# Kernel tuning notes

Hardware: AMD Instinct MI355X
Metric: run time of the kernel (lower is better)

## Reference

```python
import jax, jax.numpy as jnp
import numpy as np

BN_EPS = 1e-5


def setup_inputs() -> dict:
    key = jax.random.key(0)
    ks = jax.random.split(key, 10)
    N, E, D = 100000, 1600000, 64
    node_feats = jax.random.normal(ks[0], (N, D), dtype=jnp.float32)
    edge_feats = jax.random.randint(ks[1], (E, 3), 0, 2, dtype=jnp.int64)
    edge_index = jax.random.randint(ks[2], (2, E), 0, N, dtype=jnp.int64)
    return {
        "node_feats": node_feats,
        "edge_feats": edge_feats,
        "edge_index": edge_index,
        "num_nodes": N,
        "num_edges": E,
        "eps": jnp.zeros((1,), jnp.float32),
        "bond_emb0": jax.random.normal(ks[3], (5, D), dtype=jnp.float32) * 0.05,
        "bond_emb1": jax.random.normal(ks[4], (6, D), dtype=jnp.float32) * 0.05,
        "bond_emb2": jax.random.normal(ks[5], (2, D), dtype=jnp.float32) * 0.05,
        "W1": jax.random.normal(ks[6], (2 * D, D), dtype=jnp.float32) * (1.0 / np.sqrt(D)),
        "b1": jnp.zeros((2 * D,), jnp.float32),
        "gamma": jnp.ones((2 * D,), jnp.float32),
        "beta": jnp.zeros((2 * D,), jnp.float32),
        "W2": jax.random.normal(ks[7], (D, 2 * D), dtype=jnp.float32) * (1.0 / np.sqrt(2 * D)),
        "b2": jnp.zeros((D,), jnp.float32),
    }


def reference(node_feats, edge_feats, edge_index, num_nodes, num_edges,
              eps, bond_emb0, bond_emb1, bond_emb2,
              W1, b1, gamma, beta, W2, b2):
    # BondEncoder: sum of categorical embeddings over 3 bond features -> [E, D]
    edge_emb = (bond_emb0[edge_feats[:, 0]]
                + bond_emb1[edge_feats[:, 1]]
                + bond_emb2[edge_feats[:, 2]])
    # gather source-node feats (edge_index[1]), combine, relu -> [E, D]
    message = jax.nn.relu(node_feats[edge_index[1]] + edge_emb)
    # scatter_add into target nodes (edge_index[0]) -> [N, D]
    message_reduce = jax.ops.segment_sum(message, edge_index[0], num_segments=num_nodes)
    h = (1.0 + eps) * node_feats + message_reduce  # eps shape [1] broadcasts
    # MLP: Linear -> BatchNorm1d (training-mode batch stats) -> ReLU -> Linear
    h1 = h @ W1.T + b1  # [N, 2D]
    mean = jnp.mean(h1, axis=0)
    var = jnp.mean(jnp.square(h1 - mean), axis=0)  # biased variance (torch BN)
    h1 = gamma * (h1 - mean) * jax.lax.rsqrt(var + BN_EPS) + beta
    h1 = jax.nn.relu(h1)
    return h1 @ W2.T + b2  # [N, D]
```

## Files before the change

kernel.cpp:

```cpp
#include <hip/hip_runtime.h>
#include <stdint.h>

#define D   64
#define D2  128
#define R   196
#define NBK 512
#define CAP 4096

__global__ void k_embsum(
    const float* __restrict__ be0, const float* __restrict__ be1,
    const float* __restrict__ be2, float* __restrict__ embsum)
{
    int c = blockIdx.x;
    int t = threadIdx.x;
    int f0 = c / 12;
    int r  = c % 12;
    int f1 = r / 2;
    int f2 = r % 2;
    embsum[c * D + t] = be0[f0 * D + t] + be1[f1 * D + t] + be2[f2 * D + t];
}

__global__ void k_init(int* __restrict__ bcursor)
{
    int i = blockIdx.x * 256 + threadIdx.x;
    if (i < NBK) bcursor[i * 16] = i * CAP;
}

__global__ __launch_bounds__(256) void k_part(
    const int* __restrict__ ei, const int* __restrict__ ef,
    int* __restrict__ bcursor, int* __restrict__ payload, int E)
{
    __shared__ int scnt[NBK];
    __shared__ int sstart[NBK];
    __shared__ int sgbase[NBK];
    __shared__ int sdat[2048];
    __shared__ unsigned short sbkt[2048];
    __shared__ int sred2[256];

    int t = threadIdx.x;
    for (int i = t; i < NBK; i += 256) scnt[i] = 0;
    __syncthreads();

    int base2 = blockIdx.x * 1024;

    int b0[4], p0[4], r0[4];
    int b1[4], p1[4], r1[4];

    #pragma unroll
    for (int k = 0; k < 4; k++) {
        int i2 = base2 + k * 256 + t;
        int e0 = i2 * 2;
        if (e0 < E) {
            int2 d  = ((const int2*)ei)[i2];
            int2 s  = ((const int2*)(ei + E))[i2];
            int2 q0 = ((const int2*)ef)[3 * i2 + 0];
            int2 q1 = ((const int2*)ef)[3 * i2 + 1];
            int2 q2 = ((const int2*)ef)[3 * i2 + 2];
            {
                int bb = d.x / R; if (bb > NBK - 1) bb = NBK - 1;
                int ld = d.x - bb * R;
                int code = q0.x * 12 + q0.y * 2 + q1.x;
                b0[k] = bb;
                p0[k] = s.x | (code << 17) | (ld << 23);
                r0[k] = atomicAdd(&scnt[bb], 1);
            }
            if (e0 + 1 < E) {
                int bb = d.y / R; if (bb > NBK - 1) bb = NBK - 1;
                int ld = d.y - bb * R;
                int code = q1.y * 12 + q2.x * 2 + q2.y;
                b1[k] = bb;
                p1[k] = s.y | (code << 17) | (ld << 23);
                r1[k] = atomicAdd(&scnt[bb], 1);
            }
        }
    }
    __syncthreads();

    int c0 = scnt[t * 2], c1 = scnt[t * 2 + 1];
    sred2[t] = c0 + c1;
    __syncthreads();
    int sv = sred2[t];
    for (int off = 1; off < 256; off <<= 1) {
        int x = (t >= off) ? sred2[t - off] : 0;
        __syncthreads();
        sred2[t] += x;
        __syncthreads();
    }
    int excl = sred2[t] - sv;
    sstart[t * 2]     = excl;
    sstart[t * 2 + 1] = excl + c0;
    __syncthreads();

    for (int i = t; i < NBK; i += 256) {
        int c = scnt[i];
        if (c) sgbase[i] = atomicAdd(&bcursor[i * 16], c);
    }
    __syncthreads();

    #pragma unroll
    for (int k = 0; k < 4; k++) {
        int i2 = base2 + k * 256 + t;
        int e0 = i2 * 2;
        if (e0 < E) {
            int slot = sstart[b0[k]] + r0[k];
            sdat[slot] = p0[k]; sbkt[slot] = (unsigned short)b0[k];
            if (e0 + 1 < E) {
                slot = sstart[b1[k]] + r1[k];
                sdat[slot] = p1[k]; sbkt[slot] = (unsigned short)b1[k];
            }
        }
    }
    __syncthreads();

    int tc = E - base2 * 2; if (tc > 2048) tc = 2048;
    #pragma unroll
    for (int k = 0; k < 8; k++) {
        int i = k * 256 + t;
        if (i < tc) {
            int bb = sbkt[i];
            int pos = sgbase[bb] + (i - sstart[bb]);
            if (pos < (bb + 1) * CAP) payload[pos] = sdat[i];
        }
    }
}

__global__ __launch_bounds__(512) void k_sortred(
    const float* __restrict__ nf,
    const int* __restrict__ bcursor,
    const int* __restrict__ payload,
    const float* __restrict__ embsum,
    const float* __restrict__ epsp,
    float* __restrict__ h, int N)
{
    __shared__ float sE[60 * D];
    __shared__ int   sp[CAP];
    __shared__ int   sq[CAP];
    __shared__ int   scn[R + 1];
    __shared__ int   scur[R];
    __shared__ int   sscan[256];

    int tid = threadIdx.x;
    int b = blockIdx.x;
    int n0 = b * R;

    for (int i = tid; i < 60 * D; i += 512) sE[i] = embsum[i];
    if (tid <= R) scn[tid] = 0;
    __syncthreads();

    int js = b * CAP;
    int cnt = bcursor[b * 16] - js;
    if (cnt > CAP) cnt = CAP;
    if (cnt < 0) cnt = 0;

    for (int i = tid; i < cnt; i += 512) {
        int u = payload[js + i];
        sp[i] = u;
        atomicAdd(&scn[((unsigned)u >> 23) + 1], 1);
    }
    __syncthreads();

    if (tid < 256) sscan[tid] = (tid <= R) ? scn[tid] : 0;
    __syncthreads();
    for (int off = 1; off < 256; off <<= 1) {
        int x = 0;
        if (tid < 256 && tid >= off) x = sscan[tid - off];
        __syncthreads();
        if (tid < 256) sscan[tid] += x;
        __syncthreads();
    }
    if (tid <= R) {
        scn[tid] = sscan[tid];
        if (tid < R) scur[tid] = sscan[tid];
    }
    __syncthreads();

    for (int i = tid; i < cnt; i += 512) {
        int u = sp[i];
        int pos = atomicAdd(&scur[(unsigned)u >> 23], 1);
        sq[pos] = u;
    }
    __syncthreads();

    int w = tid >> 6, l = tid & 63;
    float epsv = 1.0f + epsp[0];
    for (int r = w; r < R; r += 8) {
        int n = n0 + r;
        if (n >= N) break;
        int st = scn[r], en = scn[r + 1];
        float acc = 0.0f;
        for (int jb = st; jb < en; jb += 64) {
            int u = (jb + l < en) ? sq[jb + l] : 0;
            int m = en - jb; if (m > 64) m = 64;
            int t = 0;
            for (; t + 4 <= m; t += 4) {
                int a0 = __shfl(u, t + 0);
                int a1 = __shfl(u, t + 1);
                int a2 = __shfl(u, t + 2);
                int a3 = __shfl(u, t + 3);
                float x0 = nf[(size_t)(a0 & 0x1FFFF) * D + l];
                float x1 = nf[(size_t)(a1 & 0x1FFFF) * D + l];
                float x2 = nf[(size_t)(a2 & 0x1FFFF) * D + l];
                float x3 = nf[(size_t)(a3 & 0x1FFFF) * D + l];
                float e0 = sE[((a0 >> 17) & 63) * D + l];
                float e1 = sE[((a1 >> 17) & 63) * D + l];
                float e2 = sE[((a2 >> 17) & 63) * D + l];
                float e3 = sE[((a3 >> 17) & 63) * D + l];
                acc += fmaxf(x0 + e0, 0.0f) + fmaxf(x1 + e1, 0.0f)
                     + fmaxf(x2 + e2, 0.0f) + fmaxf(x3 + e3, 0.0f);
            }
            for (; t < m; t++) {
                int a = __shfl(u, t);
                acc += fmaxf(nf[(size_t)(a & 0x1FFFF) * D + l]
                             + sE[((a >> 17) & 63) * D + l], 0.0f);
            }
        }
        h[(size_t)n * D + l] = fmaf(epsv, nf[(size_t)n * D + l], acc);
    }
}

__global__ __launch_bounds__(256) void k_stats(
    const float* __restrict__ h,
    float* __restrict__ pM,
    int N, int tiles)
{
    __shared__ float sH[64 * 68];
    __shared__ float sred[4 * 64];
    int tid = threadIdx.x;
    int iB = tid >> 4, jB = tid & 15;
    int rg = tid >> 6, lc = tid & 63;

    float M[4][4];
    #pragma unroll
    for (int a = 0; a < 4; a++)
        #pragma unroll
        for (int b = 0; b < 4; b++) M[a][b] = 0.0f;
    float sp = 0.0f;

    for (int t = blockIdx.x; t < tiles; t += gridDim.x) {
        int row0 = t * 64;
        __syncthreads();
        {
            int r = tid >> 2, c16 = (tid & 3) * 16;
            int gr = row0 + r;
            float* dp = &sH[r * 68 + c16];
            if (gr < N) {
                const float4* hr = (const float4*)(h + (size_t)gr * D + c16);
                #pragma unroll
                for (int m2 = 0; m2 < 4; m2++) ((float4*)dp)[m2] = hr[m2];
            } else {
                #pragma unroll
                for (int m2 = 0; m2 < 16; m2++) dp[m2] = 0.0f;
            }
        }
        __syncthreads();

        #pragma unroll 8
        for (int n2 = 0; n2 < 64; n2++) {
            float4 a = *(const float4*)&sH[n2 * 68 + iB * 4];
            float4 b = *(const float4*)&sH[n2 * 68 + jB * 4];
            M[0][0] = fmaf(a.x, b.x, M[0][0]);
            M[0][1] = fmaf(a.x, b.y, M[0][1]);
            M[0][2] = fmaf(a.x, b.z, M[0][2]);
            M[0][3] = fmaf(a.x, b.w, M[0][3]);
            M[1][0] = fmaf(a.y, b.x, M[1][0]);
            M[1][1] = fmaf(a.y, b.y, M[1][1]);
            M[1][2] = fmaf(a.y, b.z, M[1][2]);
            M[1][3] = fmaf(a.y, b.w, M[1][3]);
            M[2][0] = fmaf(a.z, b.x, M[2][0]);
            M[2][1] = fmaf(a.z, b.y, M[2][1]);
            M[2][2] = fmaf(a.z, b.z, M[2][2]);
            M[2][3] = fmaf(a.z, b.w, M[2][3]);
            M[3][0] = fmaf(a.w, b.x, M[3][0]);
            M[3][1] = fmaf(a.w, b.y, M[3][1]);
            M[3][2] = fmaf(a.w, b.z, M[3][2]);
            M[3][3] = fmaf(a.w, b.w, M[3][3]);
        }
        #pragma unroll
        for (int r2 = 0; r2 < 16; r2++)
            sp += sH[(rg * 16 + r2) * 68 + lc];
    }

    float* P = pM + (size_t)blockIdx.x * 4160;
    #pragma unroll
    for (int a = 0; a < 4; a++)
        #pragma unroll
        for (int b = 0; b < 4; b++)
            P[(iB * 4 + a) * 64 + jB * 4 + b] = M[a][b];
    sred[rg * 64 + lc] = sp;
    __syncthreads();
    if (tid < 64)
        P[4096 + tid] = sred[tid] + sred[64 + tid] + sred[128 + tid] + sred[192 + tid];
}

__global__ __launch_bounds__(256) void k_redM(
    const float* __restrict__ pM, int nblk,
    float* __restrict__ Mbar, float invN)
{
    __shared__ float sred[256];
    int tid = threadIdx.x;
    int eq = tid & 63, bq = tid >> 6;
    int e = blockIdx.x * 64 + eq;

    float s0 = 0.0f, s1 = 0.0f, s2 = 0.0f, s3 = 0.0f;
    if (e < 4160) {
        int b = bq;
        for (; b + 12 < nblk; b += 16) {
            s0 += pM[(size_t)(b +  0) * 4160 + e];
            s1 += pM[(size_t)(b +  4) * 4160 + e];
            s2 += pM[(size_t)(b +  8) * 4160 + e];
            s3 += pM[(size_t)(b + 12) * 4160 + e];
        }
        for (; b < nblk; b += 4) s0 += pM[(size_t)b * 4160 + e];
    }
    sred[tid] = (s0 + s1) + (s2 + s3);
    __syncthreads();
    if (tid < 64 && e < 4160)
        Mbar[e] = (sred[tid] + sred[64 + tid] + sred[128 + tid] + sred[192 + tid]) * invN;
}

__global__ void k_bn(
    const float* __restrict__ Mbar,
    const float* __restrict__ W1,
    const float* __restrict__ b1,
    const float* __restrict__ gamma, const float* __restrict__ beta,
    float* __restrict__ ss)
{
    __shared__ float sMb[4160];
    int tid = threadIdx.x;
    for (int i = tid; i < 4160; i += 128) sMb[i] = Mbar[i];
    __syncthreads();

    int c = tid;
    float w[64];
    #pragma unroll
    for (int k = 0; k < 64; k++) w[k] = W1[c * D + k];

    float d = 0.0f;
    #pragma unroll
    for (int k = 0; k < 64; k++) d = fmaf(w[k], sMb[4096 + k], d);

    float Q = 0.0f;
    for (int k = 0; k < 64; k++) {
        float tk = 0.0f;
        #pragma unroll
        for (int j = 0; j < 64; j++) tk = fmaf(sMb[k * 64 + j], w[j], tk);
        Q = fmaf(w[k], tk, Q);
    }

    float var  = fmaxf(Q - d * d, 0.0f);
    float mean = d + b1[c];
    float sc   = gamma[c] * rsqrtf(var + 1e-5f);
    ss[c]       = sc;
    ss[128 + c] = beta[c] - mean * sc;
}

__global__ __launch_bounds__(256) void k_gemm2(
    const float* __restrict__ h,
    const float* __restrict__ W1,
    const float* __restrict__ b1,
    const float* __restrict__ ss,
    const float* __restrict__ W2,
    const float* __restrict__ b2v,
    float* __restrict__ out,
    int N, int tiles)
{
    __shared__ float AB[32 * 128];
    __shared__ float W1t[64 * 128];
    __shared__ float W2t[128 * 64];

    int tid = threadIdx.x;
    int ty = tid >> 5, tx = tid & 31;

    {
        int c  = tid >> 1;
        int k0 = (tid & 1) * 32;
        const float4* wr = (const float4*)(W1 + c * D + k0);
        #pragma unroll
        for (int q = 0; q < 8; q++) {
            float4 u = wr[q];
            int k = k0 + q * 4;
            W1t[(k + 0) * 128 + c] = u.x;
            W1t[(k + 1) * 128 + c] = u.y;
            W1t[(k + 2) * 128 + c] = u.z;
            W1t[(k + 3) * 128 + c] = u.w;
        }
    }
    {
        int j  = tid >> 2;
        int k0 = (tid & 3) * 32;
        const float4* wr = (const float4*)(W2 + j * D2 + k0);
        #pragma unroll
        for (int q = 0; q < 8; q++) {
            float4 u = wr[q];
            int k = k0 + q * 4;
            W2t[(k + 0) * 64 + j] = u.x;
            W2t[(k + 1) * 64 + j] = u.y;
            W2t[(k + 2) * 64 + j] = u.z;
            W2t[(k + 3) * 64 + j] = u.w;
        }
    }

    float bb0 = b1[tx * 4 + 0];
    float bb1 = b1[tx * 4 + 1];
    float bb2 = b1[tx * 4 + 2];
    float bb3 = b1[tx * 4 + 3];
    float4 scv = *(const float4*)&ss[tx * 4];
    float4 shv = *(const float4*)&ss[128 + tx * 4];
    float ob0 = b2v[tx * 2 + 0];
    float ob1 = b2v[tx * 2 + 1];

    for (int t = blockIdx.x; t < tiles; t += gridDim.x) {
        int row0 = t * 32;
        __syncthreads();
        {
            int r  = tid >> 3;
            int c8 = (tid & 7) * 8;
            int gr = row0 + r;
            float* dstp = &AB[r * 128 + c8];
            if (gr < N) {
                const float4* hrow = (const float4*)(h + (size_t)gr * D + c8);
                ((float4*)dstp)[0] = hrow[0];
                ((float4*)dstp)[1] = hrow[1];
            } else {
                #pragma unroll
                for (int m = 0; m < 8; m++) dstp[m] = 0.0f;
            }
        }
        __syncthreads();

        float acc[4][4];
        #pragma unroll
        for (int i = 0; i < 4; i++)
            #pragma unroll
            for (int j = 0; j < 4; j++) acc[i][j] = 0.0f;

        #pragma unroll 4
        for (int k4 = 0; k4 < 16; k4++) {
            float4 w0 = *(const float4*)&W1t[(k4 * 4 + 0) * 128 + tx * 4];
            float4 w1 = *(const float4*)&W1t[(k4 * 4 + 1) * 128 + tx * 4];
            float4 w2 = *(const float4*)&W1t[(k4 * 4 + 2) * 128 + tx * 4];
            float4 w3 = *(const float4*)&W1t[(k4 * 4 + 3) * 128 + tx * 4];
            #pragma unroll
            for (int i = 0; i < 4; i++) {
                float4 a = *(const float4*)&AB[(ty * 4 + i) * 128 + k4 * 4];
                acc[i][0] = fmaf(a.x, w0.x, acc[i][0]);
                acc[i][1] = fmaf(a.x, w0.y, acc[i][1]);
                acc[i][2] = fmaf(a.x, w0.z, acc[i][2]);
                acc[i][3] = fmaf(a.x, w0.w, acc[i][3]);
                acc[i][0] = fmaf(a.y, w1.x, acc[i][0]);
                acc[i][1] = fmaf(a.y, w1.y, acc[i][1]);
                acc[i][2] = fmaf(a.y, w1.z, acc[i][2]);
                acc[i][3] = fmaf(a.y, w1.w, acc[i][3]);
                acc[i][0] = fmaf(a.z, w2.x, acc[i][0]);
                acc[i][1] = fmaf(a.z, w2.y, acc[i][1]);
                acc[i][2] = fmaf(a.z, w2.z, acc[i][2]);
                acc[i][3] = fmaf(a.z, w2.w, acc[i][3]);
                acc[i][0] = fmaf(a.w, w3.x, acc[i][0]);
                acc[i][1] = fmaf(a.w, w3.y, acc[i][1]);
                acc[i][2] = fmaf(a.w, w3.z, acc[i][2]);
                acc[i][3] = fmaf(a.w, w3.w, acc[i][3]);
            }
        }
        __syncthreads();

        #pragma unroll
        for (int i = 0; i < 4; i++) {
            float g0 = fmaxf(fmaf(acc[i][0] + bb0, scv.x, shv.x), 0.0f);
            float g1 = fmaxf(fmaf(acc[i][1] + bb1, scv.y, shv.y), 0.0f);
            float g2 = fmaxf(fmaf(acc[i][2] + bb2, scv.z, shv.z), 0.0f);
            float g3 = fmaxf(fmaf(acc[i][3] + bb3, scv.w, shv.w), 0.0f);
            *(float4*)&AB[(ty * 4 + i) * 128 + tx * 4] = make_float4(g0, g1, g2, g3);
        }
        __syncthreads();

        float acc2[4][2];
        #pragma unroll
        for (int i = 0; i < 4; i++) { acc2[i][0] = 0.0f; acc2[i][1] = 0.0f; }

        #pragma unroll 4
        for (int k4 = 0; k4 < 32; k4++) {
            float2 u0 = *(const float2*)&W2t[(k4 * 4 + 0) * 64 + tx * 2];
            float2 u1 = *(const float2*)&W2t[(k4 * 4 + 1) * 64 + tx * 2];
            float2 u2 = *(const float2*)&W2t[(k4 * 4 + 2) * 64 + tx * 2];
            float2 u3 = *(const float2*)&W2t[(k4 * 4 + 3) * 64 + tx * 2];
            #pragma unroll
            for (int i = 0; i < 4; i++) {
                float4 b = *(const float4*)&AB[(ty * 4 + i) * 128 + k4 * 4];
                acc2[i][0] = fmaf(b.x, u0.x, acc2[i][0]);
                acc2[i][1] = fmaf(b.x, u0.y, acc2[i][1]);
                acc2[i][0] = fmaf(b.y, u1.x, acc2[i][0]);
                acc2[i][1] = fmaf(b.y, u1.y, acc2[i][1]);
                acc2[i][0] = fmaf(b.z, u2.x, acc2[i][0]);
                acc2[i][1] = fmaf(b.z, u2.y, acc2[i][1]);
                acc2[i][0] = fmaf(b.w, u3.x, acc2[i][0]);
                acc2[i][1] = fmaf(b.w, u3.y, acc2[i][1]);
            }
        }

        #pragma unroll
        for (int i = 0; i < 4; i++) {
            int gr = row0 + ty * 4 + i;
            if (gr < N) {
                float2 pk = make_float2(acc2[i][0] + ob0, acc2[i][1] + ob1);
                ((float2*)out)[(size_t)gr * 32 + tx] = pk;
            }
        }
    }
}

extern "C" void kernel_launch(void* const* d_in, const int* in_sizes, int n_in,
                              void* d_out, int out_size, void* d_ws, size_t ws_size,
                              hipStream_t stream)
{
    const float* nf    = (const float*)d_in[0];
    const int*   ef    = (const int*)d_in[1];
    const int*   ei    = (const int*)d_in[2];
    const float* epsp  = (const float*)d_in[5];
    const float* be0   = (const float*)d_in[6];
    const float* be1   = (const float*)d_in[7];
    const float* be2   = (const float*)d_in[8];
    const float* W1    = (const float*)d_in[9];
    const float* b1    = (const float*)d_in[10];
    const float* gamma = (const float*)d_in[11];
    const float* beta  = (const float*)d_in[12];
    const float* W2    = (const float*)d_in[13];
    const float* b2v   = (const float*)d_in[14];
    float*       out   = (float*)d_out;

    int N = in_sizes[0] / D;
    int E = in_sizes[1] / 3;

    int gS = 512;
    int tilesS = (N + 63) / 64;
    int tiles2 = (N + 31) / 32;
    int g2 = 512;

    float* h       = (float*)d_ws;
    float* Mbar    = h + (size_t)N * D;
    float* ss      = Mbar + 4160;
    float* embsum  = ss + 256;
    int*   bcursor = (int*)(embsum + 60 * D);
    int*   payload = bcursor + NBK * 16;
    float* pM      = (float*)payload;

    k_init<<<2, 256, 0, stream>>>(bcursor);
    k_embsum<<<60, 64, 0, stream>>>(be0, be1, be2, embsum);

    int E2 = (E + 1) / 2;
    int gP = (E2 + 1023) / 1024;
    k_part<<<gP, 256, 0, stream>>>(ei, ef, bcursor, payload, E);

    k_sortred<<<NBK, 512, 0, stream>>>(nf, bcursor, payload, embsum, epsp, h, N);

    k_stats<<<gS, 256, 0, stream>>>(h, pM, N, tilesS);
    k_redM<<<65, 256, 0, stream>>>(pM, gS, Mbar, 1.0f / (float)N);
    k_bn<<<1, 128, 0, stream>>>(Mbar, W1, b1, gamma, beta, ss);

    k_gemm2<<<g2, 256, 0, stream>>>(h, W1, b1, ss, W2, b2v, out, N, tiles2);
}
```

Baseline: 377.9 us.

## Fuse BN second-moment stats into sort-reduce kernel and merge init launch

Removes the separate k_stats kernel: each k_sortred block now re-reads its 196 freshly written h rows into a shared-memory buffer aliased over its existing scratch, then computes the partial Gram matrix and column sums. The partials are written into that block's payload region, which is why CAP grows to 4224 so it can hold 4160 floats. The k_init launch is also folded into k_embsum as extra blocks. This saves two launches and a full extra pass over h from global memory, at the cost of a longer tail in k_sortred where only 320 of its 512 threads do the stats work.

```diff
diff --git a/kernel.cpp b/kernel.cpp
--- a/kernel.cpp
+++ b/kernel.cpp
@@ -5,25 +5,25 @@
 #define D2  128
 #define R   196
 #define NBK 512
-#define CAP 4096
+#define CAP 4224
 
 __global__ void k_embsum(
     const float* __restrict__ be0, const float* __restrict__ be1,
-    const float* __restrict__ be2, float* __restrict__ embsum)
+    const float* __restrict__ be2, float* __restrict__ embsum,
+    int* __restrict__ bcursor)
 {
     int c = blockIdx.x;
     int t = threadIdx.x;
-    int f0 = c / 12;
-    int r  = c % 12;
-    int f1 = r / 2;
-    int f2 = r % 2;
-    embsum[c * D + t] = be0[f0 * D + t] + be1[f1 * D + t] + be2[f2 * D + t];
-}
-
-__global__ void k_init(int* __restrict__ bcursor)
-{
-    int i = blockIdx.x * 256 + threadIdx.x;
-    if (i < NBK) bcursor[i * 16] = i * CAP;
+    if (c < 60) {
+        int f0 = c / 12;
+        int r  = c % 12;
+        int f1 = r / 2;
+        int f2 = r % 2;
+        embsum[c * D + t] = be0[f0 * D + t] + be1[f1 * D + t] + be2[f2 * D + t];
+    } else {
+        int i = (c - 60) * 64 + t;
+        if (i < NBK) bcursor[i * 16] = i * CAP;
+    }
 }
 
 __global__ __launch_bounds__(256) void k_part(
@@ -124,20 +124,30 @@
     }
 }
 
+#define SME   0
+#define SMP   15360
+#define SMQ   32256
+#define SMC   49152
+#define SMU   49940
+#define SMS   50724
+#define SMEM_BYTES 53376
+
 __global__ __launch_bounds__(512) void k_sortred(
     const float* __restrict__ nf,
     const int* __restrict__ bcursor,
-    const int* __restrict__ payload,
+    int* __restrict__ payload,
     const float* __restrict__ embsum,
     const float* __restrict__ epsp,
     float* __restrict__ h, int N)
 {
-    __shared__ float sE[60 * D];
-    __shared__ int   sp[CAP];
-    __shared__ int   sq[CAP];
-    __shared__ int   scn[R + 1];
-    __shared__ int   scur[R];
-    __shared__ int   sscan[256];
+    __shared__ __align__(16) char smem[SMEM_BYTES];
+    float* sE    = (float*)(smem + SME);
+    int*   sp    = (int*)(smem + SMP);
+    int*   sq    = (int*)(smem + SMQ);
+    int*   scn   = (int*)(smem + SMC);
+    int*   scur  = (int*)(smem + SMU);
+    int*   sscan = (int*)(smem + SMS);
+    float* hbuf  = (float*)smem;
 
     int tid = threadIdx.x;
     int b = blockIdx.x;
@@ -216,80 +226,57 @@
         }
         h[(size_t)n * D + l] = fmaf(epsv, nf[(size_t)n * D + l], acc);
     }
-}
-
-__global__ __launch_bounds__(256) void k_stats(
-    const float* __restrict__ h,
-    float* __restrict__ pM,
-    int N, int tiles)
-{
-    __shared__ float sH[64 * 68];
-    __shared__ float sred[4 * 64];
-    int tid = threadIdx.x;
-    int iB = tid >> 4, jB = tid & 15;
-    int rg = tid >> 6, lc = tid & 63;
-
-    float M[4][4];
-    #pragma unroll
-    for (int a = 0; a < 4; a++)
-        #pragma unroll
-        for (int b = 0; b < 4; b++) M[a][b] = 0.0f;
-    float sp = 0.0f;
-
-    for (int t = blockIdx.x; t < tiles; t += gridDim.x) {
-        int row0 = t * 64;
-        __syncthreads();
-        {
-            int r = tid >> 2, c16 = (tid & 3) * 16;
-            int gr = row0 + r;
-            float* dp = &sH[r * 68 + c16];
-            if (gr < N) {
-                const float4* hr = (const float4*)(h + (size_t)gr * D + c16);
-                #pragma unroll
-                for (int m2 = 0; m2 < 4; m2++) ((float4*)dp)[m2] = hr[m2];
-            } else {
-                #pragma unroll
-                for (int m2 = 0; m2 < 16; m2++) dp[m2] = 0.0f;
-            }
-        }
-        __syncthreads();
-
-        #pragma unroll 8
-        for (int n2 = 0; n2 < 64; n2++) {
-            float4 a = *(const float4*)&sH[n2 * 68 + iB * 4];
-            float4 b = *(const float4*)&sH[n2 * 68 + jB * 4];
-            M[0][0] = fmaf(a.x, b.x, M[0][0]);
-            M[0][1] = fmaf(a.x, b.y, M[0][1]);
-            M[0][2] = fmaf(a.x, b.z, M[0][2]);
-            M[0][3] = fmaf(a.x, b.w, M[0][3]);
-            M[1][0] = fmaf(a.y, b.x, M[1][0]);
-            M[1][1] = fmaf(a.y, b.y, M[1][1]);
-            M[1][2] = fmaf(a.y, b.z, M[1][2]);
-            M[1][3] = fmaf(a.y, b.w, M[1][3]);
-            M[2][0] = fmaf(a.z, b.x, M[2][0]);
-            M[2][1] = fmaf(a.z, b.y, M[2][1]);
-            M[2][2] = fmaf(a.z, b.z, M[2][2]);
-            M[2][3] = fmaf(a.z, b.w, M[2][3]);
-            M[3][0] = fmaf(a.w, b.x, M[3][0]);
-            M[3][1] = fmaf(a.w, b.y, M[3][1]);
-            M[3][2] = fmaf(a.w, b.z, M[3][2]);
-            M[3][3] = fmaf(a.w, b.w, M[3][3]);
-        }
-        #pragma unroll
-        for (int r2 = 0; r2 < 16; r2++)
-            sp += sH[(rg * 16 + r2) * 68 + lc];
-    }
-
-    float* P = pM + (size_t)blockIdx.x * 4160;
-    #pragma unroll
-    for (int a = 0; a < 4; a++)
-        #pragma unroll
-        for (int b = 0; b < 4; b++)
-            P[(iB * 4 + a) * 64 + jB * 4 + b] = M[a][b];
-    sred[rg * 64 + lc] = sp;
-    __syncthreads();
-    if (tid < 64)
-        P[4096 + tid] = sred[tid] + sred[64 + tid] + sred[128 + tid] + sred[192 + tid];
+    __syncthreads();
+
+    for (int idx = tid; idx < R * 16; idx += 512) {
+        int row = idx >> 4, q = idx & 15;
+        int n = n0 + row;
+        float4 v = make_float4(0.0f, 0.0f, 0.0f, 0.0f);
+        if (n < N) v = *(const float4*)&h[(size_t)n * D + q * 4];
+        *(float4*)&hbuf[row * 68 + q * 4] = v;
+    }
+    __syncthreads();
+
+    float* P = (float*)(payload + (size_t)b * CAP);
+    if (tid < 256) {
+        int iB = tid >> 4, jB = tid & 15;
+        float M[4][4];
+        #pragma unroll
+        for (int a = 0; a < 4; a++)
+            #pragma unroll
+            for (int c = 0; c < 4; c++) M[a][c] = 0.0f;
+        #pragma unroll 4
+        for (int n2 = 0; n2 < R; n2++) {
+            float4 a = *(const float4*)&hbuf[n2 * 68 + iB * 4];
+            float4 c = *(const float4*)&hbuf[n2 * 68 + jB * 4];
+            M[0][0] = fmaf(a.x, c.x, M[0][0]);
+            M[0][1] = fmaf(a.x, c.y, M[0][1]);
+            M[0][2] = fmaf(a.x, c.z, M[0][2]);
+            M[0][3] = fmaf(a.x, c.w, M[0][3]);
+            M[1][0] = fmaf(a.y, c.x, M[1][0]);
+            M[1][1] = fmaf(a.y, c.y, M[1][1]);
+            M[1][2] = fmaf(a.y, c.z, M[1][2]);
+            M[1][3] = fmaf(a.y, c.w, M[1][3]);
+            M[2][0] = fmaf(a.z, c.x, M[2][0]);
+            M[2][1] = fmaf(a.z, c.y, M[2][1]);
+            M[2][2] = fmaf(a.z, c.z, M[2][2]);
+            M[2][3] = fmaf(a.z, c.w, M[2][3]);
+            M[3][0] = fmaf(a.w, c.x, M[3][0]);
+            M[3][1] = fmaf(a.w, c.y, M[3][1]);
+            M[3][2] = fmaf(a.w, c.z, M[3][2]);
+            M[3][3] = fmaf(a.w, c.w, M[3][3]);
+        }
+        #pragma unroll
+        for (int a = 0; a < 4; a++)
+            #pragma unroll
+            for (int c = 0; c < 4; c++)
+                P[(iB * 4 + a) * 64 + jB * 4 + c] = M[a][c];
+    } else if (tid < 320) {
+        int lc = tid - 256;
+        float s = 0.0f;
+        for (int r2 = 0; r2 < R; r2++) s += hbuf[r2 * 68 + lc];
+        P[4096 + lc] = s;
+    }
 }
 
 __global__ __launch_bounds__(256) void k_redM(
@@ -305,12 +292,12 @@
     if (e < 4160) {
         int b = bq;
         for (; b + 12 < nblk; b += 16) {
-            s0 += pM[(size_t)(b +  0) * 4160 + e];
-            s1 += pM[(size_t)(b +  4) * 4160 + e];
-            s2 += pM[(size_t)(b +  8) * 4160 + e];
-            s3 += pM[(size_t)(b + 12) * 4160 + e];
-        }
-        for (; b < nblk; b += 4) s0 += pM[(size_t)b * 4160 + e];
+            s0 += pM[(size_t)(b +  0) * CAP + e];
+            s1 += pM[(size_t)(b +  4) * CAP + e];
+            s2 += pM[(size_t)(b +  8) * CAP + e];
+            s3 += pM[(size_t)(b + 12) * CAP + e];
+        }
+        for (; b < nblk; b += 4) s0 += pM[(size_t)b * CAP + e];
     }
     sred[tid] = (s0 + s1) + (s2 + s3);
     __syncthreads();
@@ -530,8 +517,6 @@
     int N = in_sizes[0] / D;
     int E = in_sizes[1] / 3;
 
-    int gS = 512;
-    int tilesS = (N + 63) / 64;
     int tiles2 = (N + 31) / 32;
     int g2 = 512;
 
@@ -543,8 +528,7 @@
     int*   payload = bcursor + NBK * 16;
     float* pM      = (float*)payload;
 
-    k_init<<<2, 256, 0, stream>>>(bcursor);
-    k_embsum<<<60, 64, 0, stream>>>(be0, be1, be2, embsum);
+    k_embsum<<<68, 64, 0, stream>>>(be0, be1, be2, embsum, bcursor);
 
     int E2 = (E + 1) / 2;
     int gP = (E2 + 1023) / 1024;
@@ -552,8 +536,7 @@
 
     k_sortred<<<NBK, 512, 0, stream>>>(nf, bcursor, payload, embsum, epsp, h, N);
 
-    k_stats<<<gS, 256, 0, stream>>>(h, pM, N, tilesS);
-    k_redM<<<65, 256, 0, stream>>>(pM, gS, Mbar, 1.0f / (float)N);
+    k_redM<<<65, 256, 0, stream>>>(pM, NBK, Mbar, 1.0f / (float)N);
     k_bn<<<1, 128, 0, stream>>>(Mbar, W1, b1, gamma, beta, ss);
 
     k_gemm2<<<g2, 256, 0, stream>>>(h, W1, b1, ss, W2, b2v, out, N, tiles2);
```

Measured after the change: 370.1 us. 1.02x faster.
